# Performance work log

Measured on AMD Instinct MI355X. Metric: run time of the kernel, lower is better.

## Reference

```python
import jax, jax.numpy as jnp
import numpy as np

D_MODEL = 1024
D_STATE = 16
D_CONV = 4
EXPAND = 2
D_INNER = EXPAND * D_MODEL  # 2048
DT_RANK = 64
B, L = 1, 1024


def setup_inputs() -> dict:
    key = jax.random.key(0)
    ks = jax.random.split(key, 10)
    s = 0.02
    x = jax.random.normal(ks[0], (B, L, D_MODEL), dtype=jnp.float32)
    in_proj_w = jax.random.normal(ks[1], (2 * D_INNER, D_MODEL), dtype=jnp.float32) * s
    conv_w = jax.random.normal(ks[2], (D_INNER, 1, D_CONV), dtype=jnp.float32) * s
    conv_b = jax.random.normal(ks[3], (D_INNER,), dtype=jnp.float32) * s
    x_proj_w = jax.random.normal(ks[4], (DT_RANK + 2 * D_STATE, D_INNER), dtype=jnp.float32) * s
    dt_init_std = DT_RANK ** (-0.5)
    dt_proj_w = jax.random.uniform(ks[5], (D_INNER, DT_RANK), dtype=jnp.float32,
                                   minval=-dt_init_std, maxval=dt_init_std)
    dt = jnp.exp(jax.random.uniform(ks[6], (D_INNER,), dtype=jnp.float32)
                 * (np.log(0.1) - np.log(0.001)) + np.log(0.001))
    dt = jnp.clip(dt, 1e-4, None)
    dt_proj_b = dt + jnp.log(-jnp.expm1(-dt))  # inverse softplus
    A_log = jnp.log(jnp.broadcast_to(jnp.arange(1, D_STATE + 1, dtype=jnp.float32),
                                     (D_INNER, D_STATE)))
    D = jnp.ones((D_INNER,), dtype=jnp.float32)
    out_proj_w = jax.random.normal(ks[7], (D_MODEL, D_INNER), dtype=jnp.float32) * s
    return {"x": x, "in_proj_w": in_proj_w, "conv_w": conv_w, "conv_b": conv_b,
            "x_proj_w": x_proj_w, "dt_proj_w": dt_proj_w, "dt_proj_b": dt_proj_b,
            "A_log": A_log, "D": D, "out_proj_w": out_proj_w}


def _selective_scan(u, delta, A, Bm, Cm, Dv):
    # u, delta: [b,l,d]; A: [d,n]; Bm, Cm: [b,l,n]; Dv: [d]
    deltaA = jnp.exp(jnp.einsum('bld,dn->bldn', delta, A))           # [b,l,d,n]
    deltaB_u = jnp.einsum('bld,bld,bln->bldn', delta, u, Bm)          # [b,l,d,n]
    xs = (jnp.swapaxes(deltaA, 0, 1), jnp.swapaxes(deltaB_u, 0, 1),
          jnp.swapaxes(Cm, 0, 1))  # time-major

    def step(state, inp):
        dA_t, dBu_t, C_t = inp               # [b,d,n], [b,d,n], [b,n]
        state = dA_t * state + dBu_t
        y_t = jnp.einsum('bdn,bn->bd', state, C_t)
        return state, y_t

    state0 = jnp.zeros((u.shape[0], u.shape[2], A.shape[1]), dtype=u.dtype)
    _, ys = jax.lax.scan(step, state0, xs)    # ys: [l,b,d]
    y = jnp.swapaxes(ys, 0, 1)
    return y + u * Dv


def reference(x, in_proj_w, conv_w, conv_b, x_proj_w, dt_proj_w, dt_proj_b,
              A_log, D, out_proj_w):
    b, l, _ = x.shape
    xz = x @ in_proj_w.T                      # [b,l,2*d_inner]
    xi, z = jnp.split(xz, 2, axis=-1)
    # causal depthwise conv1d (pad left d_conv-1, truncate to L)
    xc = jnp.swapaxes(xi, 1, 2)               # [b,d_inner,l]
    xc = jax.lax.conv_general_dilated(
        xc, conv_w, window_strides=(1,), padding=[(D_CONV - 1, 0)],
        dimension_numbers=('NCH', 'OIH', 'NCH'), feature_group_count=D_INNER)
    xc = xc + conv_b[None, :, None]
    xi = jax.nn.silu(jnp.swapaxes(xc, 1, 2))  # [b,l,d_inner]
    # SSM
    A = -jnp.exp(A_log)
    x_dbl = xi @ x_proj_w.T                   # [b,l,dt_rank+2n]
    delta, Bm, Cm = jnp.split(x_dbl, [DT_RANK, DT_RANK + D_STATE], axis=-1)
    delta = jax.nn.softplus(delta @ dt_proj_w.T + dt_proj_b)
    y = _selective_scan(xi, delta, A, Bm, Cm, D)
    y = y * jax.nn.silu(z)
    return y @ out_proj_w.T
```

## Files before the change

### kernel.cpp

```cpp
#include <hip/hip_runtime.h>
#include <hip/hip_bf16.h>
#include <cstdint>
#include <cstddef>


typedef __attribute__((ext_vector_type(4))) float f32x4;
typedef __attribute__((ext_vector_type(8))) short short8;

#define GLOAD_LDS16(g, l)                                                      \
  __builtin_amdgcn_global_load_lds(                                            \
      (const __attribute__((address_space(1))) void*)(g),                      \
      (__attribute__((address_space(3))) void*)(l), 16, 0, 0)

__device__ __forceinline__ unsigned short f2bf(float f) {
  union { float f; unsigned u; } v; v.f = f;
  unsigned u = v.u;
  unsigned r = (u + 0x7FFFu + ((u >> 16) & 1u)) >> 16;
  return (unsigned short)r;
}
__device__ __forceinline__ float bf2f(unsigned short u) {
  union { unsigned u; float f; } v; v.u = ((unsigned)u) << 16;
  return v.f;
}

__global__ __launch_bounds__(256) void convert2(
    const float* __restrict__ a0, unsigned short* __restrict__ o0, int n0,
    const float* __restrict__ a1, unsigned short* __restrict__ o1, int n1) {
  int i = blockIdx.x * 256 + threadIdx.x;
  int t0 = n0 >> 2, t1 = n1 >> 2;
  const float* a; unsigned short* o;
  if (i < t0) {
    a = a0; o = o0;
  } else if (i < t0 + t1) {
    i -= t0; a = a1; o = o1;
  } else return;
  float4 v = ((const float4*)a)[i];
  uint2 p;
  p.x = (unsigned)f2bf(v.x) | ((unsigned)f2bf(v.y) << 16);
  p.y = (unsigned)f2bf(v.z) | ((unsigned)f2bf(v.w) << 16);
  ((uint2*)o)[i] = p;
}

template <int AF32, int BF32, int SPLITK, int OBF>
__global__ __launch_bounds__(256) void gemm64(
    const void* __restrict__ Av, const void* __restrict__ Bv,
    void* __restrict__ Cv, int M, int N, int K) {
  __shared__ unsigned short lds[2][2][64 * 64];
  const int tid  = threadIdx.x;
  const int lane = tid & 63;
  const int w    = tid >> 6;

  const int nx = gridDim.x, ny = gridDim.y;
  int li = (blockIdx.z * ny + blockIdx.y) * nx + blockIdx.x;
  int xcd = li & 7, idx = li >> 3;
  int by = idx % ny;
  int r_ = idx / ny;
  int slab = nx >> 3;
  int bx = xcd * slab + (r_ % slab);
  int bz = r_ / slab;

  const int mBase = by * 64;
  const int nBase = bx * 64;
  const int kLen  = K / SPLITK;
  const int kBase = (SPLITK > 1) ? bz * kLen : 0;
  const int wr = (w >> 1) * 32;
  const int wc = (w & 1) * 32;
  const int wchunk = tid & 192;

  const int srow  = tid >> 2;
  const int sseg  = (tid & 3) * 16;
  const int sslot = (tid & 3) * 2;

  float4 ra[4], rb[4];

  auto loadA_f32 = [&](int k0) {
    const float* Af = (const float*)Av;
    #pragma unroll
    for (int i = 0; i < 4; ++i)
      ra[i] = *(const float4*)&Af[(size_t)(mBase + srow) * K + k0 + sseg + i * 4];
  };
  auto loadB_f32 = [&](int k0) {
    const float* Bf = (const float*)Bv;
    #pragma unroll
    for (int i = 0; i < 4; ++i)
      rb[i] = *(const float4*)&Bf[(size_t)(nBase + srow) * K + k0 + sseg + i * 4];
  };
  auto writeA_f32 = [&](int b) {
    unsigned short tmp[16];
    #pragma unroll
    for (int i = 0; i < 4; ++i) {
      tmp[i * 4 + 0] = f2bf(ra[i].x); tmp[i * 4 + 1] = f2bf(ra[i].y);
      tmp[i * 4 + 2] = f2bf(ra[i].z); tmp[i * 4 + 3] = f2bf(ra[i].w);
    }
    *(int4*)&lds[b][0][srow * 64 + ((sslot ^ (srow & 7)) * 8)] = *(int4*)&tmp[0];
    *(int4*)&lds[b][0][srow * 64 + (((sslot + 1) ^ (srow & 7)) * 8)] = *(int4*)&tmp[8];
  };
  auto writeB_f32 = [&](int b) {
    unsigned short tmp[16];
    #pragma unroll
    for (int i = 0; i < 4; ++i) {
      tmp[i * 4 + 0] = f2bf(rb[i].x); tmp[i * 4 + 1] = f2bf(rb[i].y);
      tmp[i * 4 + 2] = f2bf(rb[i].z); tmp[i * 4 + 3] = f2bf(rb[i].w);
    }
    *(int4*)&lds[b][1][srow * 64 + ((sslot ^ (srow & 7)) * 8)] = *(int4*)&tmp[0];
    *(int4*)&lds[b][1][srow * 64 + (((sslot + 1) ^ (srow & 7)) * 8)] = *(int4*)&tmp[8];
  };
  auto gloadA = [&](int b, int k0) {
    const unsigned short* Ab = (const unsigned short*)Av;
    #pragma unroll
    for (int j = 0; j < 2; ++j) {
      int chunk = tid + j * 256;
      int row = chunk >> 3, t = chunk & 7;
      int col = (t ^ (row & 7)) * 8;
      GLOAD_LDS16(&Ab[(size_t)(mBase + row) * K + k0 + col],
                  &lds[b][0][(size_t)(wchunk + j * 256) * 8]);
    }
  };
  auto gloadB = [&](int b, int k0) {
    const unsigned short* Bb = (const unsigned short*)Bv;
    #pragma unroll
    for (int j = 0; j < 2; ++j) {
      int chunk = tid + j * 256;
      int row = chunk >> 3, t = chunk & 7;
      int col = (t ^ (row & 7)) * 8;
      GLOAD_LDS16(&Bb[(size_t)(nBase + row) * K + k0 + col],
                  &lds[b][1][(size_t)(wchunk + j * 256) * 8]);
    }
  };

  f32x4 acc[2][2];
  #pragma unroll
  for (int m = 0; m < 2; ++m)
    #pragma unroll
    for (int n = 0; n < 2; ++n)
      acc[m][n] = (f32x4){0.f, 0.f, 0.f, 0.f};

  const int kIters = kLen / 64;
  if (AF32) { loadA_f32(kBase); writeA_f32(0); } else gloadA(0, kBase);
  if (BF32) { loadB_f32(kBase); writeB_f32(0); } else gloadB(0, kBase);
  __syncthreads();

  int buf = 0;
  for (int it = 0; it < kIters; ++it) {
    bool pre = (it + 1 < kIters);
    int kn = kBase + (it + 1) * 64;
    if (pre) {
      if (AF32) loadA_f32(kn); else gloadA(buf ^ 1, kn);
      if (BF32) loadB_f32(kn); else gloadB(buf ^ 1, kn);
    }
    short8 af[2][2], bfr[2][2];
    #pragma unroll
    for (int m = 0; m < 2; ++m)
      #pragma unroll
      for (int kk = 0; kk < 2; ++kk) {
        int row = wr + m * 16 + (lane & 15);
        int s = kk * 4 + (lane >> 4);
        af[m][kk] = *(const short8*)&lds[buf][0][row * 64 + ((s ^ (row & 7)) * 8)];
      }
    #pragma unroll
    for (int n = 0; n < 2; ++n)
      #pragma unroll
      for (int kk = 0; kk < 2; ++kk) {
        int row = wc + n * 16 + (lane & 15);
        int s = kk * 4 + (lane >> 4);
        bfr[n][kk] = *(const short8*)&lds[buf][1][row * 64 + ((s ^ (row & 7)) * 8)];
      }
    #pragma unroll
    for (int kk = 0; kk < 2; ++kk)
      #pragma unroll
      for (int m = 0; m < 2; ++m)
        #pragma unroll
        for (int n = 0; n < 2; ++n)
          acc[m][n] = __builtin_amdgcn_mfma_f32_16x16x32_bf16(
              af[m][kk], bfr[n][kk], acc[m][n], 0, 0, 0);
    if (pre) {
      if (AF32) writeA_f32(buf ^ 1);
      if (BF32) writeB_f32(buf ^ 1);
    }
    __syncthreads();
    buf ^= 1;
  }

  if (OBF) {
    unsigned short* Cb = (unsigned short*)Cv;
    #pragma unroll
    for (int m = 0; m < 2; ++m) {
      int row0 = mBase + wr + m * 16 + (lane >> 4) * 4;
      #pragma unroll
      for (int n = 0; n < 2; ++n) {
        int col = nBase + wc + n * 16 + (lane & 15);
        #pragma unroll
        for (int r = 0; r < 4; ++r)
          Cb[(size_t)(row0 + r) * N + col] = f2bf(acc[m][n][r]);
      }
    }
  } else {
    float* Co = (float*)Cv + (SPLITK > 1 ? (size_t)bz * M * N : (size_t)0);
    #pragma unroll
    for (int m = 0; m < 2; ++m) {
      int row0 = mBase + wr + m * 16 + (lane >> 4) * 4;
      #pragma unroll
      for (int n = 0; n < 2; ++n) {
        int col = nBase + wc + n * 16 + (lane & 15);
        #pragma unroll
        for (int r = 0; r < 4; ++r)
          Co[(size_t)(row0 + r) * N + col] = acc[m][n][r];
      }
    }
  }
}

__global__ __launch_bounds__(256) void reduce2(
    const float* __restrict__ P, float* __restrict__ out, int n4) {
  int i = blockIdx.x * 256 + threadIdx.x;
  if (i < n4) {
    f32x4 a = ((const f32x4*)P)[i];
    f32x4 b = ((const f32x4*)P)[i + n4];
    ((f32x4*)out)[i] = a + b;
  }
}

__global__ __launch_bounds__(256) void conv_silu(
    const unsigned short* __restrict__ xz_bf, const float* __restrict__ cw,
    const float* __restrict__ cb, unsigned short* __restrict__ xi_b) {
  int d0 = threadIdx.x * 8;
  int l0 = blockIdx.x * 4;
  float wgt[8][4], bias[8];
  #pragma unroll
  for (int j = 0; j < 8; ++j) {
    float4 t = *(const float4*)&cw[(d0 + j) * 4];
    wgt[j][0] = t.x; wgt[j][1] = t.y; wgt[j][2] = t.z; wgt[j][3] = t.w;
  }
  *(float4*)(bias + 0) = *(const float4*)&cb[d0];
  *(float4*)(bias + 4) = *(const float4*)&cb[d0 + 4];

  short8 rows[7];
  #pragma unroll
  for (int r = 0; r < 7; ++r) {
    int ll = l0 - 3 + r;
    if (ll >= 0)
      rows[r] = *(const short8*)&xz_bf[(size_t)ll * 4096 + d0];
    else
      rows[r] = (short8){0, 0, 0, 0, 0, 0, 0, 0};
  }
  #pragma unroll
  for (int q = 0; q < 4; ++q) {
    short8 outv;
    #pragma unroll
    for (int j = 0; j < 8; ++j) {
      float acc = bias[j];
      #pragma unroll
      for (int k = 0; k < 4; ++k)
        acc = fmaf(bf2f((unsigned short)rows[q + k][j]), wgt[j][k], acc);
      float s = acc / (1.f + __expf(-acc));
      outv[j] = (short)f2bf(s);
    }
    *(short8*)&xi_b[(size_t)(l0 + q) * 2048 + d0] = outv;
  }
}

__global__ __launch_bounds__(256) void xproj(
    const unsigned short* __restrict__ xi_b, const unsigned short* __restrict__ xw_b,
    unsigned short* __restrict__ xd_b, float* __restrict__ Bm, float* __restrict__ Cm) {
  __shared__ f32x4 red[4][64];
  int tid = threadIdx.x, lane = tid & 63, w = tid >> 6;
  int mt = blockIdx.x, nt = blockIdx.y;
  int arow = mt * 16 + (lane & 15);
  int brow = nt * 16 + (lane & 15);
  int kg = (lane >> 4) * 8;
  f32x4 acc = (f32x4){0.f, 0.f, 0.f, 0.f};
  for (int k0 = w * 512; k0 < (w + 1) * 512; k0 += 32) {
    short8 a = *(const short8*)&xi_b[(size_t)arow * 2048 + k0 + kg];
    short8 b = *(const short8*)&xw_b[(size_t)brow * 2048 + k0 + kg];
    acc = __builtin_amdgcn_mfma_f32_16x16x32_bf16(a, b, acc, 0, 0, 0);
  }
  red[w][lane] = acc;
  __syncthreads();
  if (w == 0) {
    acc = red[0][lane];
    acc += red[1][lane];
    acc += red[2][lane];
    acc += red[3][lane];
    int ocol = nt * 16 + (lane & 15);
    #pragma unroll
    for (int r = 0; r < 4; ++r) {
      int row = mt * 16 + (lane >> 4) * 4 + r;
      float v = acc[r];
      if (ocol < 64)      xd_b[row * 64 + ocol] = f2bf(v);
      else if (ocol < 80) Bm[row * 16 + (ocol - 64)] = v;
      else                Cm[row * 16 + (ocol - 80)] = v;
    }
  }
}

__device__ __forceinline__ void dt_tile(
    const unsigned short* __restrict__ xd, const unsigned short* __restrict__ dtw,
    const float* __restrict__ dtb, int c, int dblk, int lane,
    float* __restrict__ ldsD) {
  short8 afr[2][2], bfr4[4][2];
  #pragma unroll
  for (int lt = 0; lt < 2; ++lt)
    #pragma unroll
    for (int kk = 0; kk < 2; ++kk)
      afr[lt][kk] = *(const short8*)
          &xd[(size_t)(c * 32 + lt * 16 + (lane & 15)) * 64 + kk * 32 + (lane >> 4) * 8];
  #pragma unroll
  for (int dt = 0; dt < 4; ++dt)
    #pragma unroll
    for (int kk = 0; kk < 2; ++kk)
      bfr4[dt][kk] = *(const short8*)
          &dtw[(size_t)(dblk * 64 + dt * 16 + (lane & 15)) * 64 + kk * 32 + (lane >> 4) * 8];
  f32x4 acc[2][4];
  #pragma unroll
  for (int lt = 0; lt < 2; ++lt)
    #pragma unroll
    for (int dt = 0; dt < 4; ++dt)
      acc[lt][dt] = (f32x4){0.f, 0.f, 0.f, 0.f};
  #pragma unroll
  for (int kk = 0; kk < 2; ++kk)
    #pragma unroll
    for (int lt = 0; lt < 2; ++lt)
      #pragma unroll
      for (int dt = 0; dt < 4; ++dt)
        acc[lt][dt] = __builtin_amdgcn_mfma_f32_16x16x32_bf16(
            afr[lt][kk], bfr4[dt][kk], acc[lt][dt], 0, 0, 0);
  #pragma unroll
  for (int dt = 0; dt < 4; ++dt) {
    int dl_ = dt * 16 + (lane & 15);
    float bias = dtb[dblk * 64 + dl_];
    #pragma unroll
    for (int lt = 0; lt < 2; ++lt) {
      #pragma unroll
      for (int r = 0; r < 4; ++r) {
        int ll = lt * 16 + (lane >> 4) * 4 + r;
        float v = acc[lt][dt][r] + bias;
        float sp = (v > 20.f) ? v : log1pf(__expf(v));
        ldsD[ll * 64 + dl_] = sp;
      }
    }
  }
}

__global__ __launch_bounds__(64) void scan_p1(
    const unsigned short* __restrict__ xd, const unsigned short* __restrict__ dtw,
    const float* __restrict__ dtb, const unsigned short* __restrict__ xi,
    const float* __restrict__ BmG, const float* __restrict__ Alog,
    float* __restrict__ P, float* __restrict__ S) {
  __shared__ float ldsD[32 * 64];
  __shared__ unsigned short ldsU[32 * 64];
  __shared__ float ldsB[32 * 16];
  const int dblk = blockIdx.x, c = blockIdx.y;
  const int lane = threadIdx.x;
  const int d = dblk * 64 + lane;

  #pragma unroll
  for (int i = 0; i < 8; ++i)
    ldsB[lane + i * 64] = BmG[c * 512 + lane + i * 64];
  #pragma unroll
  for (int i = 0; i < 4; ++i) {
    int chunk = lane + i * 64;
    int row = chunk >> 3, c8 = chunk & 7;
    *(int4*)&ldsU[row * 64 + c8 * 8] =
        *(const int4*)&xi[(size_t)(c * 32 + row) * 2048 + dblk * 64 + c8 * 8];
  }
  dt_tile(xd, dtw, dtb, c, dblk, lane, ldsD);
  __syncthreads();

  float a[16], p[16], s[16];
  #pragma unroll
  for (int n = 0; n < 16; ++n) {
    a[n] = -__expf(Alog[d * 16 + n]);
    p[n] = 1.f; s[n] = 0.f;
  }
  for (int t = 0; t < 32; ++t) {
    float dl = ldsD[t * 64 + lane];
    float u  = bf2f(ldsU[t * 64 + lane]);
    float du = dl * u;
    float bv[16];
    *(float4*)(bv + 0)  = *(const float4*)&ldsB[t * 16 + 0];
    *(float4*)(bv + 4)  = *(const float4*)&ldsB[t * 16 + 4];
    *(float4*)(bv + 8)  = *(const float4*)&ldsB[t * 16 + 8];
    *(float4*)(bv + 12) = *(const float4*)&ldsB[t * 16 + 12];
    #pragma unroll
    for (int n = 0; n < 16; ++n) {
      float dA = __expf(dl * a[n]);
      s[n] = fmaf(dA, s[n], du * bv[n]);
      p[n] *= dA;
    }
  }
  #pragma unroll
  for (int n = 0; n < 16; ++n) {
    P[(size_t)(c * 16 + n) * 2048 + d] = p[n];
    S[(size_t)(c * 16 + n) * 2048 + d] = s[n];
  }
}

__global__ __launch_bounds__(256) void scan_p2(
    const float* __restrict__ P, const float* __restrict__ S,
    float* __restrict__ SIn) {
  int idx = blockIdx.x * 256 + threadIdx.x;
  float sin_ = 0.f;
  #pragma unroll 4
  for (int c = 0; c < 32; ++c) {
    SIn[c * 32768 + idx] = sin_;
    sin_ = fmaf(P[c * 32768 + idx], sin_, S[c * 32768 + idx]);
  }
}

__global__ __launch_bounds__(64) void scan_p3(
    const unsigned short* __restrict__ xd, const unsigned short* __restrict__ dtw,
    const float* __restrict__ dtb, const unsigned short* __restrict__ xi,
    const float* __restrict__ BmG, const float* __restrict__ CmG,
    const float* __restrict__ Alog, const float* __restrict__ Dv,
    const float* __restrict__ SIn, const unsigned short* __restrict__ xz,
    unsigned short* __restrict__ y_b) {
  __shared__ float ldsD[32 * 64];
  __shared__ unsigned short ldsU[32 * 64];
  __shared__ unsigned short ldsZ[32 * 64];
  __shared__ float ldsB[32 * 16];
  __shared__ float ldsC[32 * 16];
  const int dblk = blockIdx.x, c = blockIdx.y;
  const int lane = threadIdx.x;
  const int d = dblk * 64 + lane;

  #pragma unroll
  for (int i = 0; i < 8; ++i) {
    ldsB[lane + i * 64] = BmG[c * 512 + lane + i * 64];
    ldsC[lane + i * 64] = CmG[c * 512 + lane + i * 64];
  }
  #pragma unroll
  for (int i = 0; i < 4; ++i) {
    int chunk = lane + i * 64;
    int row = chunk >> 3, c8 = chunk & 7;
    *(int4*)&ldsU[row * 64 + c8 * 8] =
        *(const int4*)&xi[(size_t)(c * 32 + row) * 2048 + dblk * 64 + c8 * 8];
    *(int4*)&ldsZ[row * 64 + c8 * 8] =
        *(const int4*)&xz[(size_t)(c * 32 + row) * 4096 + 2048 + dblk * 64 + c8 * 8];
  }
  dt_tile(xd, dtw, dtb, c, dblk, lane, ldsD);
  __syncthreads();

  float a[16], s[16];
  #pragma unroll
  for (int n = 0; n < 16; ++n) {
    a[n] = -__expf(Alog[d * 16 + n]);
    s[n] = SIn[c * 32768 + n * 2048 + d];
  }
  float Dd = Dv[d];
  for (int t = 0; t < 32; ++t) {
    float dl = ldsD[t * 64 + lane];
    float u  = bf2f(ldsU[t * 64 + lane]);
    float du = dl * u;
    float bv[16], cv[16];
    *(float4*)(bv + 0)  = *(const float4*)&ldsB[t * 16 + 0];
    *(float4*)(bv + 4)  = *(const float4*)&ldsB[t * 16 + 4];
    *(float4*)(bv + 8)  = *(const float4*)&ldsB[t * 16 + 8];
    *(float4*)(bv + 12) = *(const float4*)&ldsB[t * 16 + 12];
    *(float4*)(cv + 0)  = *(const float4*)&ldsC[t * 16 + 0];
    *(float4*)(cv + 4)  = *(const float4*)&ldsC[t * 16 + 4];
    *(float4*)(cv + 8)  = *(const float4*)&ldsC[t * 16 + 8];
    *(float4*)(cv + 12) = *(const float4*)&ldsC[t * 16 + 12];
    float y = 0.f;
    #pragma unroll
    for (int n = 0; n < 16; ++n) {
      float dA = __expf(dl * a[n]);
      s[n] = fmaf(dA, s[n], du * bv[n]);
      y = fmaf(s[n], cv[n], y);
    }
    y = fmaf(u, Dd, y);
    float zz = bf2f(ldsZ[t * 64 + lane]);
    float sig = 1.f / (1.f + __expf(-zz));
    y *= zz * sig;
    y_b[(size_t)(c * 32 + t) * 2048 + d] = f2bf(y);
  }
}

extern "C" void kernel_launch(void* const* d_in, const int* in_sizes, int n_in,
                              void* d_out, int out_size, void* d_ws, size_t ws_size,
                              hipStream_t stream) {
  const float* x      = (const float*)d_in[0];
  const float* Win    = (const float*)d_in[1];
  const float* convw  = (const float*)d_in[2];
  const float* convb  = (const float*)d_in[3];
  const float* xprojw = (const float*)d_in[4];
  const float* dtw    = (const float*)d_in[5];
  const float* dtb    = (const float*)d_in[6];
  const float* Alog   = (const float*)d_in[7];
  const float* Dv     = (const float*)d_in[8];
  const float* Wout   = (const float*)d_in[9];
  float* out = (float*)d_out;

  char* ws = (char*)d_ws;
  size_t off = 0;
  auto alloc = [&](size_t bytes) -> void* {
    void* p = ws + off;
    off = (off + bytes + 255) & ~(size_t)255;
    return p;
  };
  unsigned short* xw_bf   = (unsigned short*)alloc((size_t)96 * 2048 * 2);
  unsigned short* dtw_bf  = (unsigned short*)alloc((size_t)2048 * 64 * 2);
  unsigned short* xz_bf   = (unsigned short*)alloc((size_t)1024 * 4096 * 2);
  unsigned short* xi_bf   = (unsigned short*)alloc((size_t)1024 * 2048 * 2);
  unsigned short* xd_bf   = (unsigned short*)alloc((size_t)1024 * 64 * 2);
  float* Bm               = (float*)alloc((size_t)1024 * 16 * 4);
  float* Cm               = (float*)alloc((size_t)1024 * 16 * 4);
  float* P                = (float*)alloc((size_t)32 * 16 * 2048 * 4);
  float* S                = (float*)alloc((size_t)32 * 16 * 2048 * 4);
  float* SIn              = (float*)alloc((size_t)32 * 16 * 2048 * 4);
  unsigned short* y_bf    = (unsigned short*)alloc((size_t)1024 * 2048 * 2);

  convert2<<<dim3(320), 256, 0, stream>>>(xprojw, xw_bf, 96 * 2048,
                                          dtw, dtw_bf, 2048 * 64);
  gemm64<1, 1, 1, 1><<<dim3(64, 16), 256, 0, stream>>>(
      x, Win, xz_bf, 1024, 4096, 1024);
  conv_silu<<<dim3(256), 256, 0, stream>>>(xz_bf, convw, convb, xi_bf);
  xproj<<<dim3(64, 6), 256, 0, stream>>>(xi_bf, xw_bf, xd_bf, Bm, Cm);
  scan_p1<<<dim3(32, 32), 64, 0, stream>>>(xd_bf, dtw_bf, dtb, xi_bf, Bm, Alog, P, S);
  scan_p2<<<dim3(128), 256, 0, stream>>>(P, S, SIn);
  scan_p3<<<dim3(32, 32), 64, 0, stream>>>(xd_bf, dtw_bf, dtb, xi_bf, Bm, Cm,
                                           Alog, Dv, SIn, xz_bf, y_bf);
  gemm64<0, 1, 2, 0><<<dim3(16, 16, 2), 256, 0, stream>>>(
      y_bf, Wout, P, 1024, 1024, 2048);
  reduce2<<<dim3(1024), 256, 0, stream>>>(P, out, 262144);
}
```

Baseline: 130.0 us.

## Pre-convert all GEMM operands to bf16 and use BK=128 async LDS loads with split-K 4

Moves the fp32-to-bf16 conversion of x, in_proj and out_proj weights out of the GEMM inner loops into a single batched grid-stride conversion kernel. Both GEMMs can then stage every operand with direct global-to-LDS loads, and the K tile grows from 64 to 128. The output projection switches to 4-way split-K with a 4-way reduction. The aim is to cut the register-staged fp32 loads and in-loop conversion and to raise per-iteration MFMA work, at the cost of an extra pass writing about 14 MB of bf16 copies, double the LDS use, and larger partial buffers.

```diff
diff --git a/kernel.cpp b/kernel.cpp
--- a/kernel.cpp
+++ b/kernel.cpp
@@ -23,29 +23,38 @@
   return v.f;
 }
 
-__global__ __launch_bounds__(256) void convert2(
+__global__ __launch_bounds__(256) void convert_all(
     const float* __restrict__ a0, unsigned short* __restrict__ o0, int n0,
-    const float* __restrict__ a1, unsigned short* __restrict__ o1, int n1) {
-  int i = blockIdx.x * 256 + threadIdx.x;
-  int t0 = n0 >> 2, t1 = n1 >> 2;
-  const float* a; unsigned short* o;
-  if (i < t0) {
-    a = a0; o = o0;
-  } else if (i < t0 + t1) {
-    i -= t0; a = a1; o = o1;
-  } else return;
-  float4 v = ((const float4*)a)[i];
-  uint2 p;
-  p.x = (unsigned)f2bf(v.x) | ((unsigned)f2bf(v.y) << 16);
-  p.y = (unsigned)f2bf(v.z) | ((unsigned)f2bf(v.w) << 16);
-  ((uint2*)o)[i] = p;
-}
-
-template <int AF32, int BF32, int SPLITK, int OBF>
+    const float* __restrict__ a1, unsigned short* __restrict__ o1, int n1,
+    const float* __restrict__ a2, unsigned short* __restrict__ o2, int n2,
+    const float* __restrict__ a3, unsigned short* __restrict__ o3, int n3,
+    const float* __restrict__ a4, unsigned short* __restrict__ o4, int n4) {
+  const float* a; unsigned short* o; int n;
+  switch (blockIdx.y) {
+    case 0: a = a0; o = o0; n = n0; break;
+    case 1: a = a1; o = o1; n = n1; break;
+    case 2: a = a2; o = o2; n = n2; break;
+    case 3: a = a3; o = o3; n = n3; break;
+    default: a = a4; o = o4; n = n4; break;
+  }
+  int n4c = n >> 2;
+  int stride = gridDim.x * blockDim.x;
+  for (int i = blockIdx.x * blockDim.x + threadIdx.x; i < n4c; i += stride) {
+    float4 v = ((const float4*)a)[i];
+    uint2 p;
+    p.x = (unsigned)f2bf(v.x) | ((unsigned)f2bf(v.y) << 16);
+    p.y = (unsigned)f2bf(v.z) | ((unsigned)f2bf(v.w) << 16);
+    ((uint2*)o)[i] = p;
+  }
+}
+
+template <int BK, int SPLITK, int OBF>
 __global__ __launch_bounds__(256) void gemm64(
-    const void* __restrict__ Av, const void* __restrict__ Bv,
+    const unsigned short* __restrict__ A, const unsigned short* __restrict__ B,
     void* __restrict__ Cv, int M, int N, int K) {
-  __shared__ unsigned short lds[2][2][64 * 64];
+  constexpr int NS = BK / 8;
+  constexpr int KS = BK / 32;
+  __shared__ unsigned short lds[2][2][64 * BK];
   const int tid  = threadIdx.x;
   const int lane = tid & 63;
   const int w    = tid >> 6;
@@ -65,66 +74,18 @@
   const int kBase = (SPLITK > 1) ? bz * kLen : 0;
   const int wr = (w >> 1) * 32;
   const int wc = (w & 1) * 32;
-  const int wchunk = tid & 192;
-
-  const int srow  = tid >> 2;
-  const int sseg  = (tid & 3) * 16;
-  const int sslot = (tid & 3) * 2;
-
-  float4 ra[4], rb[4];
-
-  auto loadA_f32 = [&](int k0) {
-    const float* Af = (const float*)Av;
-    #pragma unroll
-    for (int i = 0; i < 4; ++i)
-      ra[i] = *(const float4*)&Af[(size_t)(mBase + srow) * K + k0 + sseg + i * 4];
-  };
-  auto loadB_f32 = [&](int k0) {
-    const float* Bf = (const float*)Bv;
-    #pragma unroll
-    for (int i = 0; i < 4; ++i)
-      rb[i] = *(const float4*)&Bf[(size_t)(nBase + srow) * K + k0 + sseg + i * 4];
-  };
-  auto writeA_f32 = [&](int b) {
-    unsigned short tmp[16];
-    #pragma unroll
-    for (int i = 0; i < 4; ++i) {
-      tmp[i * 4 + 0] = f2bf(ra[i].x); tmp[i * 4 + 1] = f2bf(ra[i].y);
-      tmp[i * 4 + 2] = f2bf(ra[i].z); tmp[i * 4 + 3] = f2bf(ra[i].w);
-    }
-    *(int4*)&lds[b][0][srow * 64 + ((sslot ^ (srow & 7)) * 8)] = *(int4*)&tmp[0];
-    *(int4*)&lds[b][0][srow * 64 + (((sslot + 1) ^ (srow & 7)) * 8)] = *(int4*)&tmp[8];
-  };
-  auto writeB_f32 = [&](int b) {
-    unsigned short tmp[16];
-    #pragma unroll
-    for (int i = 0; i < 4; ++i) {
-      tmp[i * 4 + 0] = f2bf(rb[i].x); tmp[i * 4 + 1] = f2bf(rb[i].y);
-      tmp[i * 4 + 2] = f2bf(rb[i].z); tmp[i * 4 + 3] = f2bf(rb[i].w);
-    }
-    *(int4*)&lds[b][1][srow * 64 + ((sslot ^ (srow & 7)) * 8)] = *(int4*)&tmp[0];
-    *(int4*)&lds[b][1][srow * 64 + (((sslot + 1) ^ (srow & 7)) * 8)] = *(int4*)&tmp[8];
-  };
-  auto gloadA = [&](int b, int k0) {
-    const unsigned short* Ab = (const unsigned short*)Av;
-    #pragma unroll
-    for (int j = 0; j < 2; ++j) {
+
+  auto stage = [&](int b, int k0) {
+    #pragma unroll
+    for (int j = 0; j < NS / 4; ++j) {
       int chunk = tid + j * 256;
-      int row = chunk >> 3, t = chunk & 7;
-      int col = (t ^ (row & 7)) * 8;
-      GLOAD_LDS16(&Ab[(size_t)(mBase + row) * K + k0 + col],
-                  &lds[b][0][(size_t)(wchunk + j * 256) * 8]);
-    }
-  };
-  auto gloadB = [&](int b, int k0) {
-    const unsigned short* Bb = (const unsigned short*)Bv;
-    #pragma unroll
-    for (int j = 0; j < 2; ++j) {
-      int chunk = tid + j * 256;
-      int row = chunk >> 3, t = chunk & 7;
-      int col = (t ^ (row & 7)) * 8;
-      GLOAD_LDS16(&Bb[(size_t)(nBase + row) * K + k0 + col],
-                  &lds[b][1][(size_t)(wchunk + j * 256) * 8]);
+      int row = chunk / NS;
+      int t = chunk % NS;
+      int col = (t ^ (row & (NS - 1))) * 8;
+      GLOAD_LDS16(&A[(size_t)(mBase + row) * K + k0 + col],
+                  &lds[b][0][((size_t)(w * 64 + j * 256)) * 8]);
+      GLOAD_LDS16(&B[(size_t)(nBase + row) * K + k0 + col],
+                  &lds[b][1][((size_t)(w * 64 + j * 256)) * 8]);
     }
   };
 
@@ -135,48 +96,39 @@
     for (int n = 0; n < 2; ++n)
       acc[m][n] = (f32x4){0.f, 0.f, 0.f, 0.f};
 
-  const int kIters = kLen / 64;
-  if (AF32) { loadA_f32(kBase); writeA_f32(0); } else gloadA(0, kBase);
-  if (BF32) { loadB_f32(kBase); writeB_f32(0); } else gloadB(0, kBase);
+  const int kIters = kLen / BK;
+  stage(0, kBase);
   __syncthreads();
-
   int buf = 0;
   for (int it = 0; it < kIters; ++it) {
-    bool pre = (it + 1 < kIters);
-    int kn = kBase + (it + 1) * 64;
-    if (pre) {
-      if (AF32) loadA_f32(kn); else gloadA(buf ^ 1, kn);
-      if (BF32) loadB_f32(kn); else gloadB(buf ^ 1, kn);
-    }
-    short8 af[2][2], bfr[2][2];
+    if (it + 1 < kIters) stage(buf ^ 1, kBase + (it + 1) * BK);
+    short8 af[2][KS], bfr[2][KS];
     #pragma unroll
     for (int m = 0; m < 2; ++m)
       #pragma unroll
-      for (int kk = 0; kk < 2; ++kk) {
+      for (int kk = 0; kk < KS; ++kk) {
         int row = wr + m * 16 + (lane & 15);
         int s = kk * 4 + (lane >> 4);
-        af[m][kk] = *(const short8*)&lds[buf][0][row * 64 + ((s ^ (row & 7)) * 8)];
+        af[m][kk] = *(const short8*)
+            &lds[buf][0][row * BK + ((s ^ (row & (NS - 1))) * 8)];
       }
     #pragma unroll
     for (int n = 0; n < 2; ++n)
       #pragma unroll
-      for (int kk = 0; kk < 2; ++kk) {
+      for (int kk = 0; kk < KS; ++kk) {
         int row = wc + n * 16 + (lane & 15);
         int s = kk * 4 + (lane >> 4);
-        bfr[n][kk] = *(const short8*)&lds[buf][1][row * 64 + ((s ^ (row & 7)) * 8)];
+        bfr[n][kk] = *(const short8*)
+            &lds[buf][1][row * BK + ((s ^ (row & (NS - 1))) * 8)];
       }
     #pragma unroll
-    for (int kk = 0; kk < 2; ++kk)
+    for (int kk = 0; kk < KS; ++kk)
       #pragma unroll
       for (int m = 0; m < 2; ++m)
         #pragma unroll
         for (int n = 0; n < 2; ++n)
           acc[m][n] = __builtin_amdgcn_mfma_f32_16x16x32_bf16(
               af[m][kk], bfr[n][kk], acc[m][n], 0, 0, 0);
-    if (pre) {
-      if (AF32) writeA_f32(buf ^ 1);
-      if (BF32) writeB_f32(buf ^ 1);
-    }
     __syncthreads();
     buf ^= 1;
   }
@@ -210,13 +162,15 @@
   }
 }
 
-__global__ __launch_bounds__(256) void reduce2(
+__global__ __launch_bounds__(256) void reduce4(
     const float* __restrict__ P, float* __restrict__ out, int n4) {
   int i = blockIdx.x * 256 + threadIdx.x;
   if (i < n4) {
     f32x4 a = ((const f32x4*)P)[i];
     f32x4 b = ((const f32x4*)P)[i + n4];
-    ((f32x4*)out)[i] = a + b;
+    f32x4 c = ((const f32x4*)P)[i + 2 * n4];
+    f32x4 d = ((const f32x4*)P)[i + 3 * n4];
+    ((f32x4*)out)[i] = (a + b) + (c + d);
   }
 }
 
@@ -497,6 +451,9 @@
     off = (off + bytes + 255) & ~(size_t)255;
     return p;
   };
+  unsigned short* x_bf    = (unsigned short*)alloc((size_t)1024 * 1024 * 2);
+  unsigned short* Win_bf  = (unsigned short*)alloc((size_t)4096 * 1024 * 2);
+  unsigned short* Wout_bf = (unsigned short*)alloc((size_t)1024 * 2048 * 2);
   unsigned short* xw_bf   = (unsigned short*)alloc((size_t)96 * 2048 * 2);
   unsigned short* dtw_bf  = (unsigned short*)alloc((size_t)2048 * 64 * 2);
   unsigned short* xz_bf   = (unsigned short*)alloc((size_t)1024 * 4096 * 2);
@@ -508,18 +465,23 @@
   float* S                = (float*)alloc((size_t)32 * 16 * 2048 * 4);
   float* SIn              = (float*)alloc((size_t)32 * 16 * 2048 * 4);
   unsigned short* y_bf    = (unsigned short*)alloc((size_t)1024 * 2048 * 2);
-
-  convert2<<<dim3(320), 256, 0, stream>>>(xprojw, xw_bf, 96 * 2048,
-                                          dtw, dtw_bf, 2048 * 64);
-  gemm64<1, 1, 1, 1><<<dim3(64, 16), 256, 0, stream>>>(
-      x, Win, xz_bf, 1024, 4096, 1024);
+  float* part4            = (float*)alloc((size_t)4 * 1024 * 1024 * 4);
+
+  convert_all<<<dim3(512, 5), 256, 0, stream>>>(
+      x, x_bf, 1024 * 1024,
+      Win, Win_bf, 4096 * 1024,
+      Wout, Wout_bf, 1024 * 2048,
+      xprojw, xw_bf, 96 * 2048,
+      dtw, dtw_bf, 2048 * 64);
+  gemm64<128, 1, 1><<<dim3(64, 16), 256, 0, stream>>>(
+      x_bf, Win_bf, xz_bf, 1024, 4096, 1024);
   conv_silu<<<dim3(256), 256, 0, stream>>>(xz_bf, convw, convb, xi_bf);
   xproj<<<dim3(64, 6), 256, 0, stream>>>(xi_bf, xw_bf, xd_bf, Bm, Cm);
   scan_p1<<<dim3(32, 32), 64, 0, stream>>>(xd_bf, dtw_bf, dtb, xi_bf, Bm, Alog, P, S);
   scan_p2<<<dim3(128), 256, 0, stream>>>(P, S, SIn);
   scan_p3<<<dim3(32, 32), 64, 0, stream>>>(xd_bf, dtw_bf, dtb, xi_bf, Bm, Cm,
                                            Alog, Dv, SIn, xz_bf, y_bf);
-  gemm64<0, 1, 2, 0><<<dim3(16, 16, 2), 256, 0, stream>>>(
-      y_bf, Wout, P, 1024, 1024, 2048);
-  reduce2<<<dim3(1024), 256, 0, stream>>>(P, out, 262144);
-}
+  gemm64<128, 4, 0><<<dim3(16, 16, 4), 256, 0, stream>>>(
+      y_bf, Wout_bf, part4, 1024, 1024, 2048);
+  reduce4<<<dim3(1024), 256, 0, stream>>>(part4, out, 262144);
+}
```

Result: faster. 119.2 us (-8.3%).
